# Kernel tuning notes

Measured on AMD Instinct MI355X. Metric: run time of the kernel, lower is better.

## Reference

```python
import jax, jax.numpy as jnp
import numpy as np

B, C, H, W, E = 32, 64, 64, 64, 8

def setup_inputs() -> dict:
    key = jax.random.key(0)
    k1, k2, k3 = jax.random.split(key, 3)
    x = jax.random.normal(k1, (B, C, H, W), dtype=jnp.float32)
    gate_w = jax.random.normal(k2, (E, C, 3, 3), dtype=jnp.float32) * 0.02
    gate_b = jnp.zeros((E,), dtype=jnp.float32)
    expert_w = jax.random.normal(k3, (E, C, C), dtype=jnp.float32) * 0.05  # per-expert 1x1 conv (out,in)
    return {"x": x, "gate_w": gate_w, "gate_b": gate_b, "expert_w": expert_w}

def reference(x, gate_w, gate_b, expert_w):
    # Gating: Conv2d(C->E, k=3, stride=1, VALID), then sum over both spatial dims -> [B, E]
    g = jax.lax.conv_general_dilated(
        x, gate_w, window_strides=(1, 1), padding='VALID',
        dimension_numbers=('NCHW', 'OIHW', 'NCHW'))
    g = g + gate_b[None, :, None, None]
    gating_code = jnp.sum(g, axis=(2, 3))                      # [B, E]
    # softmax over experts then top-1
    probs = jax.nn.softmax(gating_code, axis=1)                # [B, E]
    top1_val = jnp.max(probs, axis=1)                          # [B]
    top1_idx = jnp.argmax(probs, axis=1)                       # [B]
    onehot = jax.nn.one_hot(top1_idx, E, dtype=x.dtype)        # [B, E]
    expert_weights = top1_val[:, None] * onehot                # combine tensor squeezed, [B, E]
    dispatch = onehot                                          # bool(combine) cast back to float == one-hot
    # einsum 'bjkd,ben->ebjkd' with n=1: broadcast x to every expert slot, masked by dispatch
    expert_inputs = x[None] * dispatch.T[:, :, None, None, None]   # [E, B, C, H, W]
    # experts: per-expert bias-free 1x1 conv (C -> C)
    expert_out = jnp.einsum('ebchw,efc->ebfhw', expert_inputs, expert_w)  # [E, B, C, H, W]
    # combine: einsum 'ij, ji... -> i...'
    output = jnp.einsum('be,ebchw->bchw', expert_weights, expert_out)      # [B, C, H, W]
    return output, expert_weights
```

## Files before the change

kernel.cpp:

```cpp
#include <hip/hip_runtime.h>

typedef float f4 __attribute__((ext_vector_type(4)));
typedef short bf16x8 __attribute__((ext_vector_type(8)));
typedef float f32x4 __attribute__((ext_vector_type(4)));

#define BB 32
#define CC 64
#define EE 8
#define HWX 4096
#define PXT 128

__device__ __forceinline__ unsigned bf16r(float f) {
  unsigned u = __builtin_bit_cast(unsigned, f);
  u += 0x7FFFu + ((u >> 16) & 1u);
  return u >> 16;
}
__device__ __forceinline__ unsigned pack2(float a, float b) {
  return bf16r(a) | (bf16r(b) << 16);
}

union frag_cast { bf16x8 v; unsigned u[4]; };

__global__ __launch_bounds__(256) void k_gate_sums(
    const float* __restrict__ x, const float* __restrict__ gate_w,
    float* __restrict__ gpart) {
  __shared__ float sg[9];
  __shared__ float cor[4][4];
  __shared__ float sS[9];
  int t = threadIdx.x;
  int bc = blockIdx.x;
  int c = bc & 63;
  const float* plane = x + (size_t)bc * HWX;
  int h = t >> 2, q = t & 3;
  const f4* rp = (const f4*)(plane + h * 64 + q * 16);
  f4 a0 = rp[0], a1 = rp[1], a2 = rp[2], a3 = rp[3];
  float local = (a0[0]+a0[1]+a0[2]+a0[3]) + (a1[0]+a1[1]+a1[2]+a1[3])
              + (a2[0]+a2[1]+a2[2]+a2[3]) + (a3[0]+a3[1]+a3[2]+a3[3]);
  if (t < 9) sg[t] = 0.f;
  __syncthreads();

  bool special = (h < 2) || (h >= 62);
  int ridx = (h < 2) ? h : h - 60;

  float red = local;
  #pragma unroll
  for (int off = 32; off > 0; off >>= 1) red += __shfl_down(red, off, 64);
  if ((t & 63) == 0) atomicAdd(&sg[0], red);

  if (special) atomicAdd(&sg[1 + ridx], local);
  if (q == 0) {
    atomicAdd(&sg[5], a0[0]); atomicAdd(&sg[6], a0[1]);
    if (special) { cor[ridx][0] = a0[0]; cor[ridx][1] = a0[1]; }
  }
  if (q == 3) {
    atomicAdd(&sg[7], a3[2]); atomicAdd(&sg[8], a3[3]);
    if (special) { cor[ridx][2] = a3[2]; cor[ridx][3] = a3[3]; }
  }
  __syncthreads();

  if (t == 0) {
    const int EX[3][2] = {{2,3},{0,3},{0,1}};
    float T = sg[0];
    #pragma unroll
    for (int i = 0; i < 3; i++)
      #pragma unroll
      for (int j = 0; j < 3; j++) {
        float Re = sg[1 + EX[i][0]] + sg[1 + EX[i][1]];
        float Ce = sg[5 + EX[j][0]] + sg[5 + EX[j][1]];
        float Xc = cor[EX[i][0]][EX[j][0]] + cor[EX[i][0]][EX[j][1]]
                 + cor[EX[i][1]][EX[j][0]] + cor[EX[i][1]][EX[j][1]];
        sS[i * 3 + j] = T - Re - Ce + Xc;
      }
  }
  __syncthreads();

  if (t < EE) {
    const float* gw = gate_w + ((size_t)t * CC + c) * 9;
    float ge = 0.f;
    #pragma unroll
    for (int k = 0; k < 9; k++) ge += gw[k] * sS[k];
    int b = bc >> 6;
    gpart[b * (EE * CC) + t * CC + c] = ge;
  }
}

__global__ __launch_bounds__(256) void k_mix(
    const float* __restrict__ x, const float* __restrict__ expert_w,
    const float* __restrict__ gpart, const float* __restrict__ gate_b,
    float* __restrict__ out, float* __restrict__ ew_out) {
  __shared__ float gsh[EE];
  int t = threadIdx.x;
  int pt = blockIdx.x;
  int b  = blockIdx.y;

  {
    int e = t >> 5, j = t & 31;
    const float* gp = gpart + b * (EE * CC) + e * CC;
    float gval = gp[j] + gp[j + 32];
    #pragma unroll
    for (int off = 16; off > 0; off >>= 1) gval += __shfl_down(gval, off, 32);
    if (j == 0) gsh[e] = gval + 3844.0f * gate_b[e];
  }
  __syncthreads();

  float g[EE];
  #pragma unroll
  for (int e = 0; e < EE; e++) g[e] = gsh[e];
  int best = 0; float bg = g[0];
  #pragma unroll
  for (int e = 1; e < EE; e++) if (g[e] > bg) { bg = g[e]; best = e; }
  float s = 0.f;
  #pragma unroll
  for (int e = 0; e < EE; e++) s += __expf(g[e] - bg);
  float sc = 1.0f / s;
  if (pt == 0 && t < EE) ew_out[b * EE + t] = (t == best) ? sc : 0.f;

  int wave = t >> 6;
  int lane = t & 63;
  int l15  = lane & 15;
  int quad = lane >> 4;

  const float* Wg = expert_w + (size_t)best * (CC * CC);
  bf16x8 afr[4][2];
  #pragma unroll
  for (int ft = 0; ft < 4; ft++) {
    const float* wrow = Wg + (ft * 16 + l15) * CC + quad * 8;
    #pragma unroll
    for (int kk = 0; kk < 2; kk++) {
      f4 w0 = *(const f4*)(wrow + kk * 32);
      f4 w1 = *(const f4*)(wrow + kk * 32 + 4);
      frag_cast fc;
      fc.u[0] = pack2(w0[0], w0[1]); fc.u[1] = pack2(w0[2], w0[3]);
      fc.u[2] = pack2(w1[0], w1[1]); fc.u[3] = pack2(w1[2], w1[3]);
      afr[ft][kk] = fc.v;
    }
  }

  const float* Xb = x + (size_t)b * CC * HWX + pt * PXT + 32 * wave;
  f32x4 acc[2][4] = {};
  #pragma unroll
  for (int ss = 0; ss < 2; ss++) {
    const float* xp = Xb + ss * 16 + l15 + (size_t)(quad * 8) * HWX;
    #pragma unroll
    for (int kk = 0; kk < 2; kk++) {
      const float* xq = xp + (size_t)(kk * 32) * HWX;
      float e0 = xq[0];
      float e1 = xq[HWX];
      float e2 = xq[2 * HWX];
      float e3 = xq[3 * HWX];
      float e4 = xq[4 * HWX];
      float e5 = xq[5 * HWX];
      float e6 = xq[6 * HWX];
      float e7 = xq[7 * HWX];
      frag_cast fb;
      fb.u[0] = pack2(e0, e1); fb.u[1] = pack2(e2, e3);
      fb.u[2] = pack2(e4, e5); fb.u[3] = pack2(e6, e7);
      #pragma unroll
      for (int ft = 0; ft < 4; ft++)
        acc[ss][ft] = __builtin_amdgcn_mfma_f32_16x16x32_bf16(
            afr[ft][kk], fb.v, acc[ss][ft], 0, 0, 0);
    }
  }

  #pragma unroll
  for (int ss = 0; ss < 2; ss++) {
    #pragma unroll
    for (int ft = 0; ft < 4; ft++) {
      int f = ft * 16 + quad * 4;
      float* Og = out + ((size_t)(b * CC + f)) * HWX
                + pt * PXT + 32 * wave + ss * 16 + l15;
      #pragma unroll
      for (int r = 0; r < 4; r++)
        Og[(size_t)r * HWX] = sc * acc[ss][ft][r];
    }
  }
}

extern "C" void kernel_launch(void* const* d_in, const int* in_sizes, int n_in,
                              void* d_out, int out_size, void* d_ws, size_t ws_size,
                              hipStream_t stream) {
  const float* x        = (const float*)d_in[0];
  const float* gate_w   = (const float*)d_in[1];
  const float* gate_b   = (const float*)d_in[2];
  const float* expert_w = (const float*)d_in[3];
  float* out = (float*)d_out;
  float* ew_out = out + (size_t)BB * CC * HWX;

  float* gpart = (float*)d_ws;

  k_gate_sums<<<BB * CC, 256, 0, stream>>>(x, gate_w, gpart);
  k_mix<<<dim3(HWX / PXT, BB), 256, 0, stream>>>(x, expert_w, gpart, gate_b,
                                                 out, ew_out);
}
```

Measured before the change: 102.8 us.

## Fuse gating and expert mix into one cooperative kernel with LDS-resident x tile

Replaces the two-kernel pipeline with a single cooperative kernel. Each block loads its 128-pixel by 64-channel x tile into shared memory once, computes partial gating contributions per tile, and waits at a grid-wide sync. It then reduces the gating sums, selects the top-1 expert and runs the MFMA mix from shared memory, so x is read from DRAM once instead of twice. The cost is the grid barrier and a requirement that all 1024 blocks be co-resident; if the cooperative launch fails, the old two-kernel path runs.

```diff
diff --git a/kernel.cpp b/kernel.cpp
--- a/kernel.cpp
+++ b/kernel.cpp
@@ -1,4 +1,7 @@
 #include <hip/hip_runtime.h>
+#include <hip/hip_cooperative_groups.h>
+
+namespace cg = cooperative_groups;
 
 typedef float f4 __attribute__((ext_vector_type(4)));
 typedef short bf16x8 __attribute__((ext_vector_type(8)));
@@ -9,6 +12,7 @@
 #define EE 8
 #define HWX 4096
 #define PXT 128
+#define SX 132
 
 __device__ __forceinline__ unsigned bf16r(float f) {
   unsigned u = __builtin_bit_cast(unsigned, f);
@@ -18,8 +22,180 @@
 __device__ __forceinline__ unsigned pack2(float a, float b) {
   return bf16r(a) | (bf16r(b) << 16);
 }
-
 union frag_cast { bf16x8 v; unsigned u[4]; };
+
+__global__ __launch_bounds__(256, 4) void k_fused(
+    const float* __restrict__ x, const float* __restrict__ gate_w,
+    const float* __restrict__ gate_b, const float* __restrict__ expert_w,
+    float* __restrict__ out, float* __restrict__ ew_out,
+    float* __restrict__ gcontrib) {
+  __shared__ __align__(16) float xt[CC * SX];
+  __shared__ float pT[CC];
+  __shared__ float rp4[CC][4];
+  __shared__ float cA[CC][4];
+  __shared__ float cB[CC][4];
+  __shared__ float gsh[EE];
+
+  int t = threadIdx.x;
+  int blk = blockIdx.x;
+  int b = blk >> 5, pt = blk & 31;
+  const float* Xg = x + (size_t)b * CC * HWX + pt * PXT;
+
+  ((float*)rp4)[t] = 0.f;
+
+  int g = t & 31, u = t >> 5;
+  f4 v[8];
+  #pragma unroll
+  for (int k = 0; k < 8; k++) {
+    int c = u + 8 * k;
+    v[k] = *(const f4*)(Xg + (size_t)c * HWX + 4 * g);
+    *(f4*)&xt[c * SX + 4 * g] = v[k];
+  }
+  __syncthreads();
+
+  #pragma unroll
+  for (int k = 0; k < 8; k++) {
+    int c = u + 8 * k;
+    float s = v[k][0] + v[k][1] + v[k][2] + v[k][3];
+    s += __shfl_down(s, 8, 16);
+    s += __shfl_down(s, 4, 16);
+    s += __shfl_down(s, 2, 16);
+    s += __shfl_down(s, 1, 16);
+    float sB = __shfl_down(s, 16, 32);
+    if (g == 0) {
+      pT[c] = s + sB;
+      if (pt == 0)  { rp4[c][0] = s; rp4[c][1] = sB; }
+      if (pt == 31) { rp4[c][2] = s; rp4[c][3] = sB; }
+      cA[c][0] = v[k][0]; cA[c][1] = v[k][1];
+    }
+    if (g == 15) { cA[c][2] = v[k][2]; cA[c][3] = v[k][3]; }
+    if (g == 16) { cB[c][0] = v[k][0]; cB[c][1] = v[k][1]; }
+    if (g == 31) { cB[c][2] = v[k][2]; cB[c][3] = v[k][3]; }
+  }
+  __syncthreads();
+
+  bool ed0 = (pt == 0), ed31 = (pt == 31);
+  float contrib0 = 0.f, contrib1 = 0.f;
+  #pragma unroll
+  for (int half = 0; half < 2; half++) {
+    int task = t + 256 * half;
+    int e = task >> 6, c = task & 63;
+    float T = pT[c];
+    float rs[4] = {rp4[c][0], rp4[c][1], rp4[c][2], rp4[c][3]};
+    float a0 = cA[c][0], a1 = cA[c][1], a2 = cA[c][2], a3 = cA[c][3];
+    float b0 = cB[c][0], b1 = cB[c][1], b2 = cB[c][2], b3 = cB[c][3];
+    float cs[4] = {a0 + b0, a1 + b1, a2 + b2, a3 + b3};
+    float crn[4][4];
+    #pragma unroll
+    for (int ri = 0; ri < 4; ri++)
+      #pragma unroll
+      for (int j = 0; j < 4; j++) crn[ri][j] = 0.f;
+    if (ed0)  { crn[0][0]=a0; crn[0][1]=a1; crn[0][2]=a2; crn[0][3]=a3;
+                crn[1][0]=b0; crn[1][1]=b1; crn[1][2]=b2; crn[1][3]=b3; }
+    if (ed31) { crn[2][0]=a0; crn[2][1]=a1; crn[2][2]=a2; crn[2][3]=a3;
+                crn[3][0]=b0; crn[3][1]=b1; crn[3][2]=b2; crn[3][3]=b3; }
+    const int EX[3][2] = {{2,3},{0,3},{0,1}};
+    const float* gw = gate_w + (size_t)(e * CC + c) * 9;
+    float acc = 0.f;
+    #pragma unroll
+    for (int i = 0; i < 3; i++)
+      #pragma unroll
+      for (int j = 0; j < 3; j++) {
+        float Re = rs[EX[i][0]] + rs[EX[i][1]];
+        float Ce = cs[EX[j][0]] + cs[EX[j][1]];
+        float Xc = crn[EX[i][0]][EX[j][0]] + crn[EX[i][0]][EX[j][1]]
+                 + crn[EX[i][1]][EX[j][0]] + crn[EX[i][1]][EX[j][1]];
+        acc += gw[i * 3 + j] * (T - Re - Ce + Xc);
+      }
+    if (half == 0) contrib0 = acc; else contrib1 = acc;
+  }
+  #pragma unroll
+  for (int off = 32; off; off >>= 1) {
+    contrib0 += __shfl_down(contrib0, off, 64);
+    contrib1 += __shfl_down(contrib1, off, 64);
+  }
+  int lane = t & 63, wv = t >> 6;
+  if (lane == 0) {
+    float* gc = gcontrib + ((size_t)(b * 32 + pt)) * EE;
+    gc[wv] = contrib0;
+    gc[wv + 4] = contrib1;
+  }
+
+  cg::this_grid().sync();
+
+  if (t < 64) {
+    int e = t & 7, ch = t >> 3;
+    const float* gc = gcontrib + (size_t)b * 256;
+    float p = gc[(ch * 4 + 0) * 8 + e] + gc[(ch * 4 + 1) * 8 + e]
+            + gc[(ch * 4 + 2) * 8 + e] + gc[(ch * 4 + 3) * 8 + e];
+    p += __shfl_down(p, 32, 64);
+    p += __shfl_down(p, 16, 64);
+    p += __shfl_down(p, 8, 64);
+    if (t < 8) gsh[t] = p + 3844.0f * gate_b[t];
+  }
+  __syncthreads();
+
+  float gg[EE];
+  #pragma unroll
+  for (int e = 0; e < EE; e++) gg[e] = gsh[e];
+  int best = 0; float bg = gg[0];
+  #pragma unroll
+  for (int e = 1; e < EE; e++) if (gg[e] > bg) { bg = gg[e]; best = e; }
+  float s = 0.f;
+  #pragma unroll
+  for (int e = 0; e < EE; e++) s += __expf(gg[e] - bg);
+  float sc = 1.0f / s;
+  if (pt == 0 && t < EE) ew_out[b * EE + t] = (t == best) ? sc : 0.f;
+
+  int l15 = lane & 15, quad = lane >> 4;
+  const float* Wg = expert_w + (size_t)best * (CC * CC);
+  bf16x8 afr[4][2];
+  #pragma unroll
+  for (int ft = 0; ft < 4; ft++) {
+    const float* wrow = Wg + (ft * 16 + l15) * CC + quad * 8;
+    #pragma unroll
+    for (int kk = 0; kk < 2; kk++) {
+      f4 w0 = *(const f4*)(wrow + kk * 32);
+      f4 w1 = *(const f4*)(wrow + kk * 32 + 4);
+      frag_cast fc;
+      fc.u[0] = pack2(w0[0], w0[1]); fc.u[1] = pack2(w0[2], w0[3]);
+      fc.u[2] = pack2(w1[0], w1[1]); fc.u[3] = pack2(w1[2], w1[3]);
+      afr[ft][kk] = fc.v;
+    }
+  }
+
+  f32x4 acc2[2][4] = {};
+  #pragma unroll
+  for (int ss = 0; ss < 2; ss++) {
+    int pxl = 32 * wv + 16 * ss + l15;
+    #pragma unroll
+    for (int kk = 0; kk < 2; kk++) {
+      int k0 = kk * 32 + quad * 8;
+      const float* xr = &xt[k0 * SX + pxl];
+      frag_cast fb;
+      fb.u[0] = pack2(xr[0],      xr[SX]);
+      fb.u[1] = pack2(xr[2 * SX], xr[3 * SX]);
+      fb.u[2] = pack2(xr[4 * SX], xr[5 * SX]);
+      fb.u[3] = pack2(xr[6 * SX], xr[7 * SX]);
+      #pragma unroll
+      for (int ft = 0; ft < 4; ft++)
+        acc2[ss][ft] = __builtin_amdgcn_mfma_f32_16x16x32_bf16(
+            afr[ft][kk], fb.v, acc2[ss][ft], 0, 0, 0);
+    }
+  }
+
+  #pragma unroll
+  for (int ss = 0; ss < 2; ss++)
+    #pragma unroll
+    for (int ft = 0; ft < 4; ft++) {
+      int f = ft * 16 + quad * 4;
+      float* Og = out + ((size_t)(b * CC + f)) * HWX
+                + pt * PXT + 32 * wv + ss * 16 + l15;
+      #pragma unroll
+      for (int r = 0; r < 4; r++)
+        Og[(size_t)r * HWX] = sc * acc2[ss][ft][r];
+    }
+}
 
 __global__ __launch_bounds__(256) void k_gate_sums(
     const float* __restrict__ x, const float* __restrict__ gate_w,
@@ -38,15 +214,12 @@
               + (a2[0]+a2[1]+a2[2]+a2[3]) + (a3[0]+a3[1]+a3[2]+a3[3]);
   if (t < 9) sg[t] = 0.f;
   __syncthreads();
-
   bool special = (h < 2) || (h >= 62);
   int ridx = (h < 2) ? h : h - 60;
-
   float red = local;
   #pragma unroll
   for (int off = 32; off > 0; off >>= 1) red += __shfl_down(red, off, 64);
   if ((t & 63) == 0) atomicAdd(&sg[0], red);
-
   if (special) atomicAdd(&sg[1 + ridx], local);
   if (q == 0) {
     atomicAdd(&sg[5], a0[0]); atomicAdd(&sg[6], a0[1]);
@@ -57,7 +230,6 @@
     if (special) { cor[ridx][2] = a3[2]; cor[ridx][3] = a3[3]; }
   }
   __syncthreads();
-
   if (t == 0) {
     const int EX[3][2] = {{2,3},{0,3},{0,1}};
     float T = sg[0];
@@ -73,7 +245,6 @@
       }
   }
   __syncthreads();
-
   if (t < EE) {
     const float* gw = gate_w + ((size_t)t * CC + c) * 9;
     float ge = 0.f;
@@ -92,7 +263,6 @@
   int t = threadIdx.x;
   int pt = blockIdx.x;
   int b  = blockIdx.y;
-
   {
     int e = t >> 5, j = t & 31;
     const float* gp = gpart + b * (EE * CC) + e * CC;
@@ -102,7 +272,6 @@
     if (j == 0) gsh[e] = gval + 3844.0f * gate_b[e];
   }
   __syncthreads();
-
   float g[EE];
   #pragma unroll
   for (int e = 0; e < EE; e++) g[e] = gsh[e];
@@ -114,12 +283,10 @@
   for (int e = 0; e < EE; e++) s += __expf(g[e] - bg);
   float sc = 1.0f / s;
   if (pt == 0 && t < EE) ew_out[b * EE + t] = (t == best) ? sc : 0.f;
-
   int wave = t >> 6;
   int lane = t & 63;
   int l15  = lane & 15;
   int quad = lane >> 4;
-
   const float* Wg = expert_w + (size_t)best * (CC * CC);
   bf16x8 afr[4][2];
   #pragma unroll
@@ -135,7 +302,6 @@
       afr[ft][kk] = fc.v;
     }
   }
-
   const float* Xb = x + (size_t)b * CC * HWX + pt * PXT + 32 * wave;
   f32x4 acc[2][4] = {};
   #pragma unroll
@@ -144,14 +310,8 @@
     #pragma unroll
     for (int kk = 0; kk < 2; kk++) {
       const float* xq = xp + (size_t)(kk * 32) * HWX;
-      float e0 = xq[0];
-      float e1 = xq[HWX];
-      float e2 = xq[2 * HWX];
-      float e3 = xq[3 * HWX];
-      float e4 = xq[4 * HWX];
-      float e5 = xq[5 * HWX];
-      float e6 = xq[6 * HWX];
-      float e7 = xq[7 * HWX];
+      float e0 = xq[0], e1 = xq[HWX], e2 = xq[2*HWX], e3 = xq[3*HWX];
+      float e4 = xq[4*HWX], e5 = xq[5*HWX], e6 = xq[6*HWX], e7 = xq[7*HWX];
       frag_cast fb;
       fb.u[0] = pack2(e0, e1); fb.u[1] = pack2(e2, e3);
       fb.u[2] = pack2(e4, e5); fb.u[3] = pack2(e6, e7);
@@ -161,7 +321,6 @@
             afr[ft][kk], fb.v, acc[ss][ft], 0, 0, 0);
     }
   }
-
   #pragma unroll
   for (int ss = 0; ss < 2; ss++) {
     #pragma unroll
@@ -186,9 +345,16 @@
   float* out = (float*)d_out;
   float* ew_out = out + (size_t)BB * CC * HWX;
 
-  float* gpart = (float*)d_ws;
-
-  k_gate_sums<<<BB * CC, 256, 0, stream>>>(x, gate_w, gpart);
-  k_mix<<<dim3(HWX / PXT, BB), 256, 0, stream>>>(x, expert_w, gpart, gate_b,
-                                                 out, ew_out);
-}
+  float* gcontrib = (float*)d_ws;
+  float* gpart    = (float*)d_ws + 16384;
+
+  void* args[] = {(void*)&x, (void*)&gate_w, (void*)&gate_b, (void*)&expert_w,
+                  (void*)&out, (void*)&ew_out, (void*)&gcontrib};
+  hipError_t err = hipLaunchCooperativeKernel(
+      (const void*)k_fused, dim3(BB * 32), dim3(256), args, 0, stream);
+  if (err != hipSuccess) {
+    k_gate_sums<<<BB * CC, 256, 0, stream>>>(x, gate_w, gpart);
+    k_mix<<<dim3(HWX / PXT, BB), 256, 0, stream>>>(x, expert_w, gpart, gate_b,
+                                                   out, ew_out);
+  }
+}
```

Result: slower. 178.8 us (+74.0%).
